# Performance work log

Hardware: AMD Instinct MI355X
Metric: run time of the kernel (lower is better)

## Reference

```python
import jax, jax.numpy as jnp
import numpy as np
import math

E = 512; V = 8192; B = 32; T = 16; L = 4; FF = 2048; NH = 8; TEMP = 1.0


def setup_inputs() -> dict:
    key = jax.random.key(0)
    ks = jax.random.split(key, 16)
    s = 0.02
    nrm = lambda k, shape, sc=s: jax.random.normal(k, shape, jnp.float32) * sc
    d = {}
    d['encoder_state'] = nrm(ks[0], (1, B, E), 1.0)
    d['special_symbol'] = nrm(ks[1], (1, 1, E))
    d['embed_weight'] = nrm(ks[2], (V, E), E ** -0.5)
    d['out_w'] = nrm(ks[3], (V, E))
    d['out_b'] = jnp.zeros((V,), jnp.float32)
    u = jax.random.uniform(ks[4], (T, B, V), jnp.float32, 1e-6, 1.0 - 1e-6)
    d['gumbel'] = -jnp.log(-jnp.log(u))
    d['sa_qkv_w'] = nrm(ks[5], (L, 3 * E, E)); d['sa_qkv_b'] = jnp.zeros((L, 3 * E), jnp.float32)
    d['sa_out_w'] = nrm(ks[6], (L, E, E)); d['sa_out_b'] = jnp.zeros((L, E), jnp.float32)
    d['ca_qkv_w'] = nrm(ks[7], (L, 3 * E, E)); d['ca_qkv_b'] = jnp.zeros((L, 3 * E), jnp.float32)
    d['ca_out_w'] = nrm(ks[8], (L, E, E)); d['ca_out_b'] = jnp.zeros((L, E), jnp.float32)
    for i in (1, 2, 3):
        d['ln%d_g' % i] = jnp.ones((L, E), jnp.float32)
        d['ln%d_b' % i] = jnp.zeros((L, E), jnp.float32)
    d['w1'] = nrm(ks[9], (L, FF, E)); d['b1'] = jnp.zeros((L, FF), jnp.float32)
    d['w2'] = nrm(ks[10], (L, E, FF)); d['b2'] = jnp.zeros((L, E), jnp.float32)
    return d


def _ln(x, g, b):
    m = x.mean(-1, keepdims=True)
    v = ((x - m) ** 2).mean(-1, keepdims=True)
    return (x - m) / jnp.sqrt(v + 1e-5) * g + b


def _mha(q_in, kv_in, qkv_w, qkv_b, out_w, out_b, mask):
    # q_in: [Sq,B,E], kv_in: [Sk,B,E]; fused PyTorch-style in_proj
    hd = E // NH
    wq, wk, wv = jnp.split(qkv_w, 3, 0)
    bq, bk, bv = jnp.split(qkv_b, 3, 0)
    q = (q_in @ wq.T + bq).reshape(q_in.shape[0], -1, NH, hd)
    k = (kv_in @ wk.T + bk).reshape(kv_in.shape[0], -1, NH, hd)
    v = (kv_in @ wv.T + bv).reshape(kv_in.shape[0], -1, NH, hd)
    s = jnp.einsum('qbhd,kbhd->bhqk', q, k) / math.sqrt(hd)
    if mask is not None:
        s = s + mask
    a = jax.nn.softmax(s, -1)
    o = jnp.einsum('bhqk,kbhd->qbhd', a, v).reshape(q_in.shape[0], -1, E)
    return o @ out_w.T + out_b


def _forward(encoder_state, special_symbol, embed_weight, out_w, out_b, gumbel,
             sa_qkv_w, sa_qkv_b, sa_out_w, sa_out_b,
             ca_qkv_w, ca_qkv_b, ca_out_w, ca_out_b,
             ln1_g, ln1_b, ln2_g, ln2_b, ln3_g, ln3_b,
             w1, b1, w2, b2):
    bsz = encoder_state.shape[1]
    embed_scale = math.sqrt(E)
    inp = jnp.broadcast_to(special_symbol, (1, bsz, E))  # special start symbol
    seq_steps, distribs = [], []
    for step in range(T):
        t = step + 1
        mask = jnp.where(jnp.triu(jnp.ones((t, t), bool), 1), -jnp.inf, 0.0)
        x = inp
        for l in range(L):  # post-norm TransformerDecoderLayer, erf-gelu
            sa = _mha(x, x, sa_qkv_w[l], sa_qkv_b[l], sa_out_w[l], sa_out_b[l], mask)
            x = _ln(x + sa, ln1_g[l], ln1_b[l])
            ca = _mha(x, encoder_state, ca_qkv_w[l], ca_qkv_b[l], ca_out_w[l], ca_out_b[l], None)
            x = _ln(x + ca, ln2_g[l], ln2_b[l])
            ff = jax.nn.gelu(x @ w1[l].T + b1[l], approximate=False) @ w2[l].T + b2[l]
            x = _ln(x + ff, ln3_g[l], ln3_b[l])
        logits = x[-1] @ out_w.T + out_b  # [B,V], last position only
        distribs.append(jax.nn.softmax(logits, -1))
        sample = jax.nn.softmax((logits + gumbel[step]) / TEMP, -1)  # gumbel-softmax (training mode)
        seq_steps.append(sample)
        new_emb = (sample @ embed_weight) * embed_scale  # soft embedding lookup
        inp = jnp.concatenate([inp, new_emb[None]], 0)
    sequence = jnp.stack(seq_steps).transpose(1, 0, 2)  # [B,T,V]
    eos = jnp.zeros_like(sequence[:, :1, :]).at[:, :, 0].set(1.0)
    sequence = jnp.concatenate([sequence, eos], 1)  # [B,T+1,V]
    return sequence, jnp.stack(distribs)  # distribs: [T,B,V]


def reference(encoder_state, special_symbol, embed_weight, out_w, out_b, gumbel,
              sa_qkv_w, sa_qkv_b, sa_out_w, sa_out_b,
              ca_qkv_w, ca_qkv_b, ca_out_w, ca_out_b,
              ln1_g, ln1_b, ln2_g, ln2_b, ln3_g, ln3_b,
              w1, b1, w2, b2):
    return _forward(encoder_state, special_symbol, embed_weight, out_w, out_b, gumbel,
                    sa_qkv_w, sa_qkv_b, sa_out_w, sa_out_b,
                    ca_qkv_w, ca_qkv_b, ca_out_w, ca_out_b,
                    ln1_g, ln1_b, ln2_g, ln2_b, ln3_g, ln3_b,
                    w1, b1, w2, b2)
```

## Files before the change

kernel.cpp:

```cpp
#include <hip/hip_runtime.h>
#include <math.h>

#define BB 32
#define EE 512
#define VV 8192
#define TT 16
#define LL 4
#define FFD 2048
#define NHD 8
#define HDD 64
#define LDP 520
#define RWP 516
#define OLP 72
#define SCALE_EMB 22.627416997969522f

typedef __attribute__((ext_vector_type(8))) short bf16x8;
typedef __attribute__((ext_vector_type(4))) float f32x4;
typedef unsigned long long ull;

__device__ __forceinline__ f32x4 mfma16(bf16x8 a, bf16x8 b, f32x4 c){
  return __builtin_amdgcn_mfma_f32_16x16x32_bf16(a, b, c, 0, 0, 0);
}

__device__ __forceinline__ float wave_sum(float v){
  for (int o = 32; o; o >>= 1) v += __shfl_down(v, o);
  return __shfl(v, 0);
}
__device__ __forceinline__ unsigned short f_to_bf(float f){
  unsigned u = __float_as_uint(f);
  unsigned r = (u + 0x7fffu + ((u >> 16) & 1u)) >> 16;
  return (unsigned short)r;
}
__device__ __forceinline__ float2 bf2_to_f2(const unsigned short* p){
  unsigned u = *(const unsigned*)p;
  float2 r;
  r.x = __uint_as_float(u << 16);
  r.y = __uint_as_float(u & 0xffff0000u);
  return r;
}
union UF { ull u; unsigned short s[4]; };
__device__ __forceinline__ ull pkbf4(float a, float b, float c, float d){
  UF x; x.s[0] = f_to_bf(a); x.s[1] = f_to_bf(b); x.s[2] = f_to_bf(c); x.s[3] = f_to_bf(d); return x.u;
}

__device__ __forceinline__ void gemm_chunk(const float* __restrict__ wrow0, int ldw,
    const unsigned short* xs, float* wt, float acc[4][2]){
  const int t = threadIdx.x, fg = t & 15, bg = t >> 4;
  #pragma unroll 1
  for (int c = 0; c < 8; ++c){
    const int k0 = c*64;
    __syncthreads();
    {
      int i = t*4;
      #pragma unroll
      for (int p = 0; p < 4; ++p, i += 1024){
        const int fr = i >> 6, kk = i & 63;
        float4 v = *(const float4*)(wrow0 + (size_t)fr*ldw + k0 + kk);
        wt[(kk+0)*68 + fr] = v.x;
        wt[(kk+1)*68 + fr] = v.y;
        wt[(kk+2)*68 + fr] = v.z;
        wt[(kk+3)*68 + fr] = v.w;
      }
    }
    __syncthreads();
    const unsigned short* xr0 = xs + (bg*2)*EE + k0;
    const unsigned short* xr1 = xr0 + EE;
    #pragma unroll 8
    for (int k = 0; k < 64; k += 2){
      float w0[4], w1[4];
      *(float4*)w0 = *(const float4*)(wt + (k+0)*68 + fg*4);
      *(float4*)w1 = *(const float4*)(wt + (k+1)*68 + fg*4);
      float2 xv0 = bf2_to_f2(xr0 + k);
      float2 xv1 = bf2_to_f2(xr1 + k);
      #pragma unroll
      for (int i = 0; i < 4; ++i){
        acc[i][0] += w0[i]*xv0.x + w1[i]*xv0.y;
        acc[i][1] += w0[i]*xv1.x + w1[i]*xv1.y;
      }
    }
  }
}

__device__ __forceinline__ void stage_x_512(unsigned short* xs,
    const float* __restrict__ xraw, const float* __restrict__ ybuf,
    const float* __restrict__ g, const float* __restrict__ bt, int use_ln,
    float* __restrict__ xlnout){
  if (!use_ln){
    for (int i = threadIdx.x*4; i < BB*EE; i += 2048){
      float4 v = *(const float4*)(xraw + i);
      int r = i >> 9, c = i & 511;
      *(ull*)(xs + r*LDP + c) = pkbf4(v.x, v.y, v.z, v.w);
    }
  } else {
    const int lane = threadIdx.x & 63, wv = threadIdx.x >> 6;
    for (int r = wv*4; r < wv*4 + 4; ++r){
      float vals[8]; float s = 0.f, s2 = 0.f;
      #pragma unroll
      for (int j = 0; j < 8; ++j){
        float v = ybuf[r*EE + lane + j*64];
        vals[j] = v; s += v; s2 += v*v;
      }
      s = wave_sum(s); s2 = wave_sum(s2);
      float m = s * (1.f/EE);
      float inv = rsqrtf(s2*(1.f/EE) - m*m + 1e-5f);
      #pragma unroll
      for (int j = 0; j < 8; ++j){
        int c = lane + j*64;
        float v = (vals[j]-m)*inv*g[c] + bt[c];
        xs[r*LDP + c] = f_to_bf(v);
        if (xlnout) xlnout[r*EE + c] = v;
      }
    }
  }
  __syncthreads();
}


__global__ __launch_bounds__(256) void k_init(const float* __restrict__ special,
    float* __restrict__ dseq, float* __restrict__ x,
    float* __restrict__ o2a, float* __restrict__ o2b,
    float* __restrict__ y0, float* __restrict__ y1){
  int idx = blockIdx.x*256 + threadIdx.x;
  if (idx < BB*VV){
    int b = idx >> 13, v = idx & (VV-1);
    dseq[(size_t)b*((TT+1)*VV) + (size_t)TT*VV + v] = (v == 0) ? 1.f : 0.f;
  } else if (idx < BB*VV + BB*EE){
    x[idx - BB*VV] = special[idx & (EE-1)];
  } else if (idx < BB*VV + 2*BB*EE){
    o2a[idx - BB*VV - BB*EE] = 0.f;
  } else if (idx < BB*VV + 3*BB*EE){
    o2b[idx - BB*VV - 2*BB*EE] = 0.f;
  } else if (idx < BB*VV + 4*BB*EE){
    y0[idx - BB*VV - 3*BB*EE] = 0.f;
  } else if (idx < BB*VV + 5*BB*EE){
    y1[idx - BB*VV - 4*BB*EE] = 0.f;
  }
}

__global__ __launch_bounds__(256) void k_penc(const float* __restrict__ enc,
    const float* __restrict__ w, const float* __restrict__ bias, float* __restrict__ venc){
  __shared__ unsigned short xs[BB*EE];
  __shared__ float wt[64*68];
  const int l = blockIdx.x >> 3, et = blockIdx.x & 7;
  for (int i = threadIdx.x; i < BB*EE; i += 256) xs[i] = f_to_bf(enc[i]);
  const int t = threadIdx.x, fg = t & 15, bg = t >> 4;
  const int f0 = et*64;
  const float* wl = w + (size_t)l*3*EE*EE + (size_t)(2*EE + f0)*EE;
  const float* bl = bias + l*3*EE + 2*EE + f0;
  float acc[4][2];
  #pragma unroll
  for (int i = 0; i < 4; ++i){ float bv = bl[fg*4+i]; acc[i][0] = bv; acc[i][1] = bv; }
  gemm_chunk(wl, EE, xs, wt, acc);
  #pragma unroll
  for (int i = 0; i < 4; ++i)
    #pragma unroll
    for (int j = 0; j < 2; ++j)
      venc[(size_t)l*BB*EE + (bg*2+j)*EE + f0 + fg*4 + i] = acc[i][j];
}

__global__ __launch_bounds__(256) void k_pca(const float* __restrict__ venc,
    const float* __restrict__ w, const float* __restrict__ bias, float* __restrict__ cac){
  __shared__ unsigned short xs[BB*EE];
  __shared__ float wt[64*68];
  const int l = blockIdx.x >> 3, et = blockIdx.x & 7;
  const float* vin = venc + (size_t)l*BB*EE;
  for (int i = threadIdx.x; i < BB*EE; i += 256) xs[i] = f_to_bf(vin[i]);
  const int t = threadIdx.x, fg = t & 15, bg = t >> 4;
  const int f0 = et*64;
  const float* wl = w + (size_t)l*EE*EE + (size_t)f0*EE;
  const float* bl = bias + l*EE + f0;
  float acc[4][2];
  #pragma unroll
  for (int i = 0; i < 4; ++i){ float bv = bl[fg*4+i]; acc[i][0] = bv; acc[i][1] = bv; }
  gemm_chunk(wl, EE, xs, wt, acc);
  #pragma unroll
  for (int i = 0; i < 4; ++i)
    #pragma unroll
    for (int j = 0; j < 2; ++j)
      cac[(size_t)l*BB*EE + (bg*2+j)*EE + f0 + fg*4 + i] = acc[i][j];
}

__global__ __launch_bounds__(256) void k_cvt(const float* __restrict__ s,
    unsigned short* __restrict__ d, int n4){
  int i = blockIdx.x*256 + threadIdx.x;
  if (i < n4){
    float4 v = ((const float4*)s)[i];
    ushort4 o;
    o.x = f_to_bf(v.x); o.y = f_to_bf(v.y); o.z = f_to_bf(v.z); o.w = f_to_bf(v.w);
    ((ushort4*)d)[i] = o;
  }
}

__global__ __launch_bounds__(256) void k_embT(const float* __restrict__ emb,
    unsigned short* __restrict__ eT){
  __shared__ unsigned short tl[64][68];
  const int vt = blockIdx.x >> 3, et = blockIdx.x & 7;
  const int v0 = vt*64, e0 = et*64;
  for (int i = threadIdx.x; i < 64*64; i += 256){
    int vv = i >> 6, ee = i & 63;
    tl[vv][ee] = f_to_bf(emb[(size_t)(v0+vv)*EE + e0 + ee]);
  }
  __syncthreads();
  for (int i = threadIdx.x; i < 64*64; i += 256){
    int ee = i >> 6, vv = i & 63;
    eT[(size_t)(e0+ee)*VV + v0 + vv] = tl[vv][ee];
  }
}


__global__ __launch_bounds__(512) void k_A(
    const float* __restrict__ x, const float* __restrict__ ybuf,
    const float* __restrict__ lng, const float* __restrict__ lnb, int use_ln,
    const unsigned short* __restrict__ Wb, const float* __restrict__ bias,
    const unsigned short* __restrict__ owb_l,
    float* __restrict__ kcl, float* __restrict__ vcl,
    float* __restrict__ xln, float* __restrict__ o2,
    int tpos, int tlen){
  __shared__ unsigned short xs[BB*LDP];
  __shared__ __align__(16) float qs[BB*68];
  __shared__ float att[BB*16];
  const int h = blockIdx.x;
  stage_x_512(xs, x, ybuf, lng, lnb, use_ln, (use_ln && h == 0) ? xln : nullptr);
  const int t = threadIdx.x, wv = t >> 6, lane = t & 63;
  const int lm = lane & 15, kg = lane >> 4;
  const unsigned short* b0r = xs + lm*LDP + kg*8;
  const unsigned short* b1r = xs + (lm+16)*LDP + kg*8;
  if (wv < 6){
    const int c = wv >> 1, half = wv & 1;
    #pragma unroll
    for (int ft = 0; ft < 2; ++ft){
      const int frel_t = (half*2 + ft)*16;
      const unsigned short* ar = Wb + (size_t)(c*EE + h*64 + frel_t + lm)*EE + kg*8;
      f32x4 acc0 = {0.f,0.f,0.f,0.f}, acc1 = {0.f,0.f,0.f,0.f};
      #pragma unroll 4
      for (int ks = 0; ks < 16; ++ks){
        bf16x8 a  = *reinterpret_cast<const bf16x8*>(ar + ks*32);
        bf16x8 b0 = *reinterpret_cast<const bf16x8*>(b0r + ks*32);
        bf16x8 b1 = *reinterpret_cast<const bf16x8*>(b1r + ks*32);
        acc0 = mfma16(a, b0, acc0);
        acc1 = mfma16(a, b1, acc1);
      }
      #pragma unroll
      for (int r = 0; r < 4; ++r){
        const int frel = frel_t + kg*4 + r;
        const float bv = bias[c*EE + h*64 + frel];
        float v0 = acc0[r] + bv, v1 = acc1[r] + bv;
        if (c == 0){
          qs[lm*68 + frel] = v0;
          qs[(lm+16)*68 + frel] = v1;
        } else if (c == 1){
          kcl[((lm*NHD + h)*TT + tpos)*HDD + frel] = v0;
          kcl[(((lm+16)*NHD + h)*TT + tpos)*HDD + frel] = v1;
        } else {
          vcl[((lm*NHD + h)*TT + tpos)*HDD + frel] = v0;
          vcl[(((lm+16)*NHD + h)*TT + tpos)*HDD + frel] = v1;
        }
      }
    }
  }
  __syncthreads();
  {
    const int b = t >> 4, j = t & 15;
    if (j < tlen){
      const float* qrow = qs + b*68;
      const float* krow = kcl + ((b*NHD + h)*TT + j)*HDD;
      float a = 0.f;
      #pragma unroll
      for (int d = 0; d < HDD; d += 4){
        float4 qv = *(const float4*)(qrow + d);
        float4 kv = *(const float4*)(krow + d);
        a += qv.x*kv.x + qv.y*kv.y + qv.z*kv.z + qv.w*kv.w;
      }
      att[b*16 + j] = a*0.125f;
    }
  }
  __syncthreads();
  if (t < 32){
    const int b = t;
    float m = -1e30f;
    for (int j = 0; j < tlen; ++j) m = fmaxf(m, att[b*16 + j]);
    float s = 0.f;
    for (int j = 0; j < tlen; ++j) s += __expf(att[b*16 + j] - m);
    float inv = 1.f/s;
    for (int j = 0; j < tlen; ++j) att[b*16 + j] = __expf(att[b*16 + j] - m)*inv;
  }
  __syncthreads();
  unsigned short* o_lds = (unsigned short*)qs;
  {
    const int b = t >> 4, d0 = (t & 15)*4;
    float acc[4];
    #pragma unroll
    for (int i = 0; i < 4; ++i) acc[i] = 0.f;
    const float* vrow = vcl + ((b*NHD + h)*TT)*HDD + d0;
    for (int j = 0; j < tlen; ++j){
      const float a = att[b*16 + j];
      float4 v = *(const float4*)(vrow + j*HDD);
      acc[0] += a*v.x; acc[1] += a*v.y; acc[2] += a*v.z; acc[3] += a*v.w;
    }
    *(ull*)(o_lds + b*OLP + d0) = pkbf4(acc[0], acc[1], acc[2], acc[3]);
  }
  __syncthreads();
  const unsigned short* ob0 = o_lds + lm*OLP + kg*8;
  const unsigned short* ob1 = o_lds + (lm+16)*OLP + kg*8;
  #pragma unroll
  for (int ft = 0; ft < 4; ++ft){
    const int f0 = wv*64 + ft*16;
    const unsigned short* ar = owb_l + (size_t)(f0 + lm)*EE + h*HDD + kg*8;
    f32x4 a0 = {0.f,0.f,0.f,0.f}, a1 = {0.f,0.f,0.f,0.f};
    #pragma unroll
    for (int ks = 0; ks < 2; ++ks){
      bf16x8 a  = *reinterpret_cast<const bf16x8*>(ar + ks*32);
      bf16x8 x0 = *reinterpret_cast<const bf16x8*>(ob0 + ks*32);
      bf16x8 x1 = *reinterpret_cast<const bf16x8*>(ob1 + ks*32);
      a0 = mfma16(a, x0, a0);
      a1 = mfma16(a, x1, a1);
    }
    #pragma unroll
    for (int r = 0; r < 4; ++r){
      const int f = f0 + kg*4 + r;
      atomicAdd(&o2[lm*EE + f], a0[r]);
      atomicAdd(&o2[(lm+16)*EE + f], a1[r]);
    }
  }
}

__global__ __launch_bounds__(512) void k_BC(
    const float* __restrict__ o2buf, const float* __restrict__ resid,
    const float* __restrict__ ob, const float* __restrict__ cac,
    const float* __restrict__ g1, const float* __restrict__ b1g,
    const float* __restrict__ g2, const float* __restrict__ b2g,
    const float* __restrict__ b2bias,
    const unsigned short* __restrict__ w1b, const float* __restrict__ b1bias,
    const unsigned short* __restrict__ w2b,
    float* __restrict__ ycur, float* __restrict__ yzero, float* __restrict__ o2zero){
  __shared__ unsigned short xs[BB*LDP];
  __shared__ __align__(16) float rawf[BB*RWP];
  __shared__ unsigned short Hs[BB*OLP];
  const int t = threadIdx.x, blk = blockIdx.x;
  for (int i = t*4; i < BB*EE; i += 2048){
    const int r = i >> 9, c = i & 511;
    float4 a  = *(const float4*)(o2buf + i);
    float4 rr = *(const float4*)(resid + i);
    float4 ov = *(const float4*)(ob + c);
    rawf[r*RWP + c]     = a.x + rr.x + ov.x;
    rawf[r*RWP + c + 1] = a.y + rr.y + ov.y;
    rawf[r*RWP + c + 2] = a.z + rr.z + ov.z;
    rawf[r*RWP + c + 3] = a.w + rr.w + ov.w;
  }
  __syncthreads();
  const int wv = t >> 6, lane = t & 63;
  const int lm = lane & 15, kg = lane >> 4;
  {
    const int c0 = lane*4, c1 = 256 + lane*4;
    for (int r = wv*4; r < wv*4 + 4; ++r){
      float v[8];
      *(float4*)(v+0) = *(const float4*)(rawf + r*RWP + c0);
      *(float4*)(v+4) = *(const float4*)(rawf + r*RWP + c1);
      float s = 0.f, s2 = 0.f;
      #pragma unroll
      for (int j = 0; j < 8; ++j){ s += v[j]; s2 += v[j]*v[j]; }
      s = wave_sum(s); s2 = wave_sum(s2);
      float m = s*(1.f/EE), inv = rsqrtf(s2*(1.f/EE) - m*m + 1e-5f);
      float4 ca0 = *(const float4*)(cac + (size_t)r*EE + c0);
      float4 ca1 = *(const float4*)(cac + (size_t)r*EE + c1);
      float nv[8]; float u = 0.f, u2 = 0.f;
      nv[0] = (v[0]-m)*inv*g1[c0+0] + b1g[c0+0] + ca0.x;
      nv[1] = (v[1]-m)*inv*g1[c0+1] + b1g[c0+1] + ca0.y;
      nv[2] = (v[2]-m)*inv*g1[c0+2] + b1g[c0+2] + ca0.z;
      nv[3] = (v[3]-m)*inv*g1[c0+3] + b1g[c0+3] + ca0.w;
      nv[4] = (v[4]-m)*inv*g1[c1+0] + b1g[c1+0] + ca1.x;
      nv[5] = (v[5]-m)*inv*g1[c1+1] + b1g[c1+1] + ca1.y;
      nv[6] = (v[6]-m)*inv*g1[c1+2] + b1g[c1+2] + ca1.z;
      nv[7] = (v[7]-m)*inv*g1[c1+3] + b1g[c1+3] + ca1.w;
      #pragma unroll
      for (int j = 0; j < 8; ++j){ u += nv[j]; u2 += nv[j]*nv[j]; }
      u = wave_sum(u); u2 = wave_sum(u2);
      float m2 = u*(1.f/EE), inv2 = rsqrtf(u2*(1.f/EE) - m2*m2 + 1e-5f);
      float o0 = (nv[0]-m2)*inv2*g2[c0+0] + b2g[c0+0];
      float o1 = (nv[1]-m2)*inv2*g2[c0+1] + b2g[c0+1];
      float o2v = (nv[2]-m2)*inv2*g2[c0+2] + b2g[c0+2];
      float o3 = (nv[3]-m2)*inv2*g2[c0+3] + b2g[c0+3];
      float o4 = (nv[4]-m2)*inv2*g2[c1+0] + b2g[c1+0];
      float o5 = (nv[5]-m2)*inv2*g2[c1+1] + b2g[c1+1];
      float o6 = (nv[6]-m2)*inv2*g2[c1+2] + b2g[c1+2];
      float o7 = (nv[7]-m2)*inv2*g2[c1+3] + b2g[c1+3];
      *(ull*)(xs + r*LDP + c0) = pkbf4(o0, o1, o2v, o3);
      *(ull*)(xs + r*LDP + c1) = pkbf4(o4, o5, o6, o7);
      if ((c0 >> 4) == blk){
        atomicAdd(&ycur[(size_t)r*EE + c0+0], o0 + b2bias[c0+0]);
        atomicAdd(&ycur[(size_t)r*EE + c0+1], o1 + b2bias[c0+1]);
        atomicAdd(&ycur[(size_t)r*EE + c0+2], o2v + b2bias[c0+2]);
        atomicAdd(&ycur[(size_t)r*EE + c0+3], o3 + b2bias[c0+3]);
      }
      if ((c1 >> 4) == blk){
        atomicAdd(&ycur[(size_t)r*EE + c1+0], o4 + b2bias[c1+0]);
        atomicAdd(&ycur[(size_t)r*EE + c1+1], o5 + b2bias[c1+1]);
        atomicAdd(&ycur[(size_t)r*EE + c1+2], o6 + b2bias[c1+2]);
        atomicAdd(&ycur[(size_t)r*EE + c1+3], o7 + b2bias[c1+3]);
      }
    }
  }
  __syncthreads();
  {
    const int ftile = wv & 3, rh = wv >> 2;
    const int f0w = blk*64 + ftile*16;
    const unsigned short* ar = w1b + (size_t)(f0w + lm)*EE + kg*8;
    const unsigned short* br = xs + (lm + rh*16)*LDP + kg*8;
    f32x4 acc = {0.f,0.f,0.f,0.f};
    #pragma unroll 4
    for (int ks = 0; ks < 16; ++ks){
      bf16x8 a = *reinterpret_cast<const bf16x8*>(ar + ks*32);
      bf16x8 b = *reinterpret_cast<const bf16x8*>(br + ks*32);
      acc = mfma16(a, b, acc);
    }
    const int fbrel = ftile*16 + kg*4;
    float hh[4];
    #pragma unroll
    for (int r = 0; r < 4; ++r){
      const float bv = b1bias[blk*64 + fbrel + r];
      float vv = acc[r] + bv;
      hh[r] = 0.5f*vv*(1.f + erff(vv*0.70710678118654752f));
    }
    *(ull*)(Hs + (lm + rh*16)*OLP + fbrel) = pkbf4(hh[0], hh[1], hh[2], hh[3]);
  }
  __syncthreads();
  {
    const unsigned short* hb0 = Hs + lm*OLP + kg*8;
    const unsigned short* hb1 = Hs + (lm+16)*OLP + kg*8;
    #pragma unroll
    for (int et = 0; et < 4; ++et){
      const int e0 = (wv*4 + et)*16;
      const unsigned short* ar = w2b + (size_t)(e0 + lm)*FFD + blk*64 + kg*8;
      f32x4 a0 = {0.f,0.f,0.f,0.f}, a1 = {0.f,0.f,0.f,0.f};
      #pragma unroll
      for (int ks = 0; ks < 2; ++ks){
        bf16x8 a  = *reinterpret_cast<const bf16x8*>(ar + ks*32);
        bf16x8 h0 = *reinterpret_cast<const bf16x8*>(hb0 + ks*32);
        bf16x8 h1 = *reinterpret_cast<const bf16x8*>(hb1 + ks*32);
        a0 = mfma16(a, h0, a0);
        a1 = mfma16(a, h1, a1);
      }
      #pragma unroll
      for (int r = 0; r < 4; ++r){
        const int e = e0 + kg*4 + r;
        atomicAdd(&ycur[lm*EE + e], a0[r]);
        atomicAdd(&ycur[(lm+16)*EE + e], a1[r]);
      }
    }
  }
  yzero[blk*512 + t] = 0.f;
  o2zero[blk*512 + t] = 0.f;
}

__global__ __launch_bounds__(512) void k_logits_m(
    const float* __restrict__ ybuf, const float* __restrict__ lng, const float* __restrict__ lnb,
    const unsigned short* __restrict__ Wb, const float* __restrict__ bias,
    float* __restrict__ logits){
  __shared__ unsigned short xs[BB*LDP];
  stage_x_512(xs, nullptr, ybuf, lng, lnb, 1, nullptr);
  const int t = threadIdx.x, wv = t >> 6, lane = t & 63;
  const int lm = lane & 15, kg = lane >> 4;
  const int ftile = wv & 3, rh = wv >> 2;
  const int f0w = blockIdx.x*64 + ftile*16;
  const unsigned short* ar = Wb + (size_t)(f0w + lm)*EE + kg*8;
  const unsigned short* br = xs + (lm + rh*16)*LDP + kg*8;
  f32x4 acc = {0.f,0.f,0.f,0.f};
  #pragma unroll 4
  for (int ks = 0; ks < 16; ++ks){
    bf16x8 a = *reinterpret_cast<const bf16x8*>(ar + ks*32);
    bf16x8 b = *reinterpret_cast<const bf16x8*>(br + ks*32);
    acc = mfma16(a, b, acc);
  }
  #pragma unroll
  for (int r = 0; r < 4; ++r){
    const int f = f0w + kg*4 + r;
    logits[(size_t)(lm + rh*16)*VV + f] = acc[r] + bias[f];
  }
}

__global__ __launch_bounds__(512) void k_softmax(const float* __restrict__ logits,
    const float* __restrict__ gum, float* __restrict__ dseq, float* __restrict__ ddist,
    unsigned short* __restrict__ sbf, float* __restrict__ x, int step){
  const int b = blockIdx.x, t = threadIdx.x, lane = t & 63, wv = t >> 6;
  __shared__ float red[16];
  const float* lr = logits + (size_t)b*VV;
  const float* gr = gum + (size_t)b*VV;
  float lv[16], gv[16];
  #pragma unroll
  for (int g4 = 0; g4 < 4; ++g4){
    const int i0 = t*4 + g4*2048;
    float4 l4 = *(const float4*)(lr + i0);
    float4 g4v = *(const float4*)(gr + i0);
    lv[g4*4+0]=l4.x; lv[g4*4+1]=l4.y; lv[g4*4+2]=l4.z; lv[g4*4+3]=l4.w;
    gv[g4*4+0]=g4v.x; gv[g4*4+1]=g4v.y; gv[g4*4+2]=g4v.z; gv[g4*4+3]=g4v.w;
  }
  float m1 = -1e30f, m2 = -1e30f;
  #pragma unroll
  for (int j = 0; j < 16; ++j){
    m1 = fmaxf(m1, lv[j]);
    m2 = fmaxf(m2, lv[j] + gv[j]);
  }
  for (int o = 32; o; o >>= 1){ m1 = fmaxf(m1, __shfl_down(m1,o)); m2 = fmaxf(m2, __shfl_down(m2,o)); }
  if (lane == 0){ red[wv] = m1; red[8+wv] = m2; }
  __syncthreads();
  m1 = red[0]; m2 = red[8];
  #pragma unroll
  for (int j = 1; j < 8; ++j){ m1 = fmaxf(m1, red[j]); m2 = fmaxf(m2, red[8+j]); }
  __syncthreads();
  float s1 = 0.f, s2 = 0.f;
  #pragma unroll
  for (int j = 0; j < 16; ++j){
    s1 += __expf(lv[j] - m1);
    s2 += __expf(lv[j] + gv[j] - m2);
  }
  for (int o = 32; o; o >>= 1){ s1 += __shfl_down(s1,o); s2 += __shfl_down(s2,o); }
  if (lane == 0){ red[wv] = s1; red[8+wv] = s2; }
  __syncthreads();
  s1 = 0.f; s2 = 0.f;
  #pragma unroll
  for (int j = 0; j < 8; ++j){ s1 += red[j]; s2 += red[8+j]; }
  float r1 = 1.f/s1, r2 = 1.f/s2;
  float* dq = dseq + (size_t)b*((TT+1)*VV) + (size_t)step*VV;
  float* dd = ddist + (size_t)b*VV;
  #pragma unroll
  for (int g4 = 0; g4 < 4; ++g4){
    const int i0 = t*4 + g4*2048;
    float4 ddv, dqv;
    ddv.x = __expf(lv[g4*4+0]-m1)*r1; ddv.y = __expf(lv[g4*4+1]-m1)*r1;
    ddv.z = __expf(lv[g4*4+2]-m1)*r1; ddv.w = __expf(lv[g4*4+3]-m1)*r1;
    dqv.x = __expf(lv[g4*4+0]+gv[g4*4+0]-m2)*r2;
    dqv.y = __expf(lv[g4*4+1]+gv[g4*4+1]-m2)*r2;
    dqv.z = __expf(lv[g4*4+2]+gv[g4*4+2]-m2)*r2;
    dqv.w = __expf(lv[g4*4+3]+gv[g4*4+3]-m2)*r2;
    *(float4*)(dd + i0) = ddv;
    *(float4*)(dq + i0) = dqv;
    *(ull*)(sbf + (size_t)b*VV + i0) = pkbf4(dqv.x, dqv.y, dqv.z, dqv.w);
  }
  x[b*EE + t] = 0.f;
}

__global__ __launch_bounds__(512) void k_embed_m(
    const unsigned short* __restrict__ eT, const unsigned short* __restrict__ sbf,
    float* __restrict__ x){
  const int t = threadIdx.x, wv = t >> 6, lane = t & 63;
  const int lm = lane & 15, kg = lane >> 4;
  const int etile = wv & 3, rh = wv >> 2;
  const int e0 = (blockIdx.x & 7)*64 + etile*16;
  const int v0 = (blockIdx.x >> 3)*512;
  const unsigned short* ar = eT + (size_t)(e0 + lm)*VV + v0 + kg*8;
  const unsigned short* br = sbf + (size_t)(lm + rh*16)*VV + v0 + kg*8;
  f32x4 acc = {0.f,0.f,0.f,0.f};
  #pragma unroll 4
  for (int ks = 0; ks < 16; ++ks){
    bf16x8 a = *reinterpret_cast<const bf16x8*>(ar + ks*32);
    bf16x8 b = *reinterpret_cast<const bf16x8*>(br + ks*32);
    acc = mfma16(a, b, acc);
  }
  #pragma unroll
  for (int r = 0; r < 4; ++r){
    const int e = e0 + kg*4 + r;
    atomicAdd(&x[(lm + rh*16)*EE + e], acc[r]*SCALE_EMB);
  }
}

extern "C" void kernel_launch(void* const* d_in, const int* in_sizes, int n_in,
                              void* d_out, int out_size, void* d_ws, size_t ws_size,
                              hipStream_t stream){
  (void)in_sizes; (void)n_in; (void)out_size; (void)ws_size;
  const float* enc  = (const float*)d_in[0];
  const float* spec = (const float*)d_in[1];
  const float* embw = (const float*)d_in[2];
  const float* outw = (const float*)d_in[3];
  const float* outb = (const float*)d_in[4];
  const float* gumb = (const float*)d_in[5];
  const float* saqw = (const float*)d_in[6];
  const float* saqb = (const float*)d_in[7];
  const float* saow = (const float*)d_in[8];
  const float* saob = (const float*)d_in[9];
  const float* caqw = (const float*)d_in[10];
  const float* caqb = (const float*)d_in[11];
  const float* caow = (const float*)d_in[12];
  const float* caob = (const float*)d_in[13];
  const float* l1g  = (const float*)d_in[14];
  const float* l1b  = (const float*)d_in[15];
  const float* l2g  = (const float*)d_in[16];
  const float* l2b  = (const float*)d_in[17];
  const float* l3g  = (const float*)d_in[18];
  const float* l3b  = (const float*)d_in[19];
  const float* w1   = (const float*)d_in[20];
  const float* b1   = (const float*)d_in[21];
  const float* w2   = (const float*)d_in[22];
  const float* b2   = (const float*)d_in[23];

  float* dout = (float*)d_out;
  float* dseq = dout;
  float* ddistbase = dout + (size_t)BB*(TT+1)*VV;

  unsigned char* p = (unsigned char*)d_ws;
  auto alloc = [&](size_t bytes) -> void* {
    void* r = (void*)p; p += (bytes + 255) & ~(size_t)255; return r;
  };
  float* x      = (float*)alloc(BB*EE*4);
  float* y0     = (float*)alloc(BB*EE*4);
  float* y1     = (float*)alloc(BB*EE*4);
  float* xln    = (float*)alloc(BB*EE*4);
  float* o2a    = (float*)alloc(BB*EE*4);
  float* o2b    = (float*)alloc(BB*EE*4);
  float* logits = (float*)alloc((size_t)BB*VV*4);
  float* venc   = (float*)alloc((size_t)LL*BB*EE*4);
  float* cac    = (float*)alloc((size_t)LL*BB*EE*4);
  float* kcache = (float*)alloc((size_t)LL*BB*EE*TT*4);
  float* vcache = (float*)alloc((size_t)LL*BB*EE*TT*4);
  unsigned short* sbf   = (unsigned short*)alloc((size_t)BB*VV*2);
  unsigned short* wqkvb = (unsigned short*)alloc((size_t)LL*3*EE*EE*2);
  unsigned short* owb   = (unsigned short*)alloc((size_t)LL*EE*EE*2);
  unsigned short* w1b   = (unsigned short*)alloc((size_t)LL*FFD*EE*2);
  unsigned short* w2b   = (unsigned short*)alloc((size_t)LL*FFD*EE*2);
  unsigned short* outwb = (unsigned short*)alloc((size_t)VV*EE*2);
  unsigned short* eTb   = (unsigned short*)alloc((size_t)EE*VV*2);

  k_init<<<1344, 256, 0, stream>>>(spec, dseq, x, o2a, o2b, y0, y1);
  k_penc<<<32, 256, 0, stream>>>(enc, caqw, caqb, venc);
  k_pca<<<32, 256, 0, stream>>>(venc, caow, caob, cac);
  k_cvt<<<(LL*3*EE*EE/4 + 255)/256, 256, 0, stream>>>(saqw, wqkvb, LL*3*EE*EE/4);
  k_cvt<<<(LL*EE*EE/4 + 255)/256, 256, 0, stream>>>(saow, owb, LL*EE*EE/4);
  k_cvt<<<(LL*FFD*EE/4 + 255)/256, 256, 0, stream>>>(w1, w1b, LL*FFD*EE/4);
  k_cvt<<<(LL*FFD*EE/4 + 255)/256, 256, 0, stream>>>(w2, w2b, LL*FFD*EE/4);
  k_cvt<<<(VV*EE/4 + 255)/256, 256, 0, stream>>>(outw, outwb, VV*EE/4);
  k_embT<<<1024, 256, 0, stream>>>(embw, eTb);

  float* yb[2]  = { y0, y1 };
  float* o2p[2] = { o2a, o2b };

  for (int step = 0; step < TT; ++step){
    const int tpos = step, tlen = step + 1;
    for (int l = 0; l < LL; ++l){
      const int use_ln = (l > 0);
      const int par = l & 1, opp = par ^ 1;
      const float* lg = l3g + (use_ln ? (l-1)*EE : 0);
      const float* lb = l3b + (use_ln ? (l-1)*EE : 0);
      float* kcl = kcache + (size_t)l*BB*EE*TT;
      float* vcl = vcache + (size_t)l*BB*EE*TT;
      k_A<<<NHD, 512, 0, stream>>>(x, yb[opp], lg, lb, use_ln,
          wqkvb + (size_t)l*3*EE*EE, saqb + (size_t)l*3*EE,
          owb + (size_t)l*EE*EE, kcl, vcl, xln, o2p[par], tpos, tlen);
      k_BC<<<32, 512, 0, stream>>>(o2p[par], use_ln ? xln : x,
          saob + (size_t)l*EE, cac + (size_t)l*BB*EE,
          l1g + l*EE, l1b + l*EE, l2g + l*EE, l2b + l*EE, b2 + l*EE,
          w1b + (size_t)l*FFD*EE, b1 + l*FFD, w2b + (size_t)l*EE*FFD,
          yb[par], yb[opp], o2p[opp]);
    }
    k_logits_m<<<128, 512, 0, stream>>>(yb[1], l3g + 3*EE, l3b + 3*EE, outwb, outb, logits);
    k_softmax<<<32, 512, 0, stream>>>(logits, gumb + (size_t)step*BB*VV, dseq,
        ddistbase + (size_t)step*BB*VV, sbf, x, step);
    k_embed_m<<<128, 512, 0, stream>>>(eTb, sbf, x);
  }
}
```

Measured before the change: 4.143 ms.

## Fuse softmax into logits and embedding kernels using unshifted exponent sums

The separate softmax kernel is removed. The logits kernel now computes exp(logit) and exp(logit+gumbel) directly, with no max subtraction, writes both to buffers and accumulates the row sums atomically. A combined kernel then normalizes, runs the soft embedding matmul, and writes the distribution and sequence outputs. Zeroing of x and gs moves into the layer kernels. This saves one launch per step and the round trip through the logits buffer, but without the max shift exp can overflow when logits are large, and global float atomics make the sums order-dependent.

```diff
diff --git a/kernel.cpp b/kernel.cpp
--- a/kernel.cpp
+++ b/kernel.cpp
@@ -215,13 +215,15 @@
     const unsigned short* __restrict__ owb_l,
     float* __restrict__ kcl, float* __restrict__ vcl,
     float* __restrict__ xln, float* __restrict__ o2,
-    int tpos, int tlen){
+    float* __restrict__ gs, int tpos, int tlen){
   __shared__ unsigned short xs[BB*LDP];
   __shared__ __align__(16) float qs[BB*68];
   __shared__ float att[BB*16];
   const int h = blockIdx.x;
+  const int t = threadIdx.x;
+  if (!use_ln && h == 0 && t < 64) gs[t] = 0.f;
   stage_x_512(xs, x, ybuf, lng, lnb, use_ln, (use_ln && h == 0) ? xln : nullptr);
-  const int t = threadIdx.x, wv = t >> 6, lane = t & 63;
+  const int wv = t >> 6, lane = t & 63;
   const int lm = lane & 15, kg = lane >> 4;
   const unsigned short* b0r = xs + lm*LDP + kg*8;
   const unsigned short* b1r = xs + (lm+16)*LDP + kg*8;
@@ -332,7 +334,8 @@
     const float* __restrict__ b2bias,
     const unsigned short* __restrict__ w1b, const float* __restrict__ b1bias,
     const unsigned short* __restrict__ w2b,
-    float* __restrict__ ycur, float* __restrict__ yzero, float* __restrict__ o2zero){
+    float* __restrict__ ycur, float* __restrict__ yzero, float* __restrict__ o2zero,
+    float* __restrict__ xz){
   __shared__ unsigned short xs[BB*LDP];
   __shared__ __align__(16) float rawf[BB*RWP];
   __shared__ unsigned short Hs[BB*OLP];
@@ -450,20 +453,74 @@
   }
   yzero[blk*512 + t] = 0.f;
   o2zero[blk*512 + t] = 0.f;
-}
-
-__global__ __launch_bounds__(512) void k_logits_m(
+  if (xz) xz[blk*512 + t] = 0.f;
+}
+
+__global__ __launch_bounds__(512) void k_logits_e(
     const float* __restrict__ ybuf, const float* __restrict__ lng, const float* __restrict__ lnb,
     const unsigned short* __restrict__ Wb, const float* __restrict__ bias,
-    float* __restrict__ logits){
+    const float* __restrict__ gum,
+    float* __restrict__ el, float* __restrict__ eg, float* __restrict__ gs){
   __shared__ unsigned short xs[BB*LDP];
+  __shared__ float ls[64];
+  const int t = threadIdx.x;
+  if (t < 64) ls[t] = 0.f;
   stage_x_512(xs, nullptr, ybuf, lng, lnb, 1, nullptr);
-  const int t = threadIdx.x, wv = t >> 6, lane = t & 63;
+  const int wv = t >> 6, lane = t & 63;
   const int lm = lane & 15, kg = lane >> 4;
   const int ftile = wv & 3, rh = wv >> 2;
   const int f0w = blockIdx.x*64 + ftile*16;
+  const int b = lm + rh*16;
   const unsigned short* ar = Wb + (size_t)(f0w + lm)*EE + kg*8;
-  const unsigned short* br = xs + (lm + rh*16)*LDP + kg*8;
+  const unsigned short* br = xs + b*LDP + kg*8;
+  f32x4 acc = {0.f,0.f,0.f,0.f};
+  #pragma unroll 4
+  for (int ks = 0; ks < 16; ++ks){
+    bf16x8 a = *reinterpret_cast<const bf16x8*>(ar + ks*32);
+    bf16x8 bb = *reinterpret_cast<const bf16x8*>(br + ks*32);
+    acc = mfma16(a, bb, acc);
+  }
+  const int fb = f0w + kg*4;
+  float4 g4 = *(const float4*)(gum + (size_t)b*VV + fb);
+  float l0 = acc[0] + bias[fb+0], l1 = acc[1] + bias[fb+1];
+  float l2 = acc[2] + bias[fb+2], l3 = acc[3] + bias[fb+3];
+  float e10 = __expf(l0), e11 = __expf(l1), e12 = __expf(l2), e13 = __expf(l3);
+  float e20 = __expf(l0+g4.x), e21 = __expf(l1+g4.y), e22 = __expf(l2+g4.z), e23 = __expf(l3+g4.w);
+  float4 ev1; ev1.x=e10; ev1.y=e11; ev1.z=e12; ev1.w=e13;
+  float4 ev2; ev2.x=e20; ev2.y=e21; ev2.z=e22; ev2.w=e23;
+  *(float4*)(el + (size_t)b*VV + fb) = ev1;
+  *(float4*)(eg + (size_t)b*VV + fb) = ev2;
+  atomicAdd(&ls[b],      e10+e11+e12+e13);
+  atomicAdd(&ls[32 + b], e20+e21+e22+e23);
+  __syncthreads();
+  if (t < 64) atomicAdd(&gs[t], ls[t]);
+}
+
+__global__ __launch_bounds__(512) void k_SMEM(
+    const unsigned short* __restrict__ eT,
+    const float* __restrict__ el, const float* __restrict__ eg,
+    const float* __restrict__ gs,
+    float* __restrict__ dseq, float* __restrict__ ddist,
+    float* __restrict__ x, int step){
+  __shared__ unsigned short ss[BB*LDP];
+  __shared__ float rr[64];
+  const int t = threadIdx.x;
+  const int et = blockIdx.x & 7, v0 = (blockIdx.x >> 3)*512;
+  if (t < 64) rr[t] = 1.f / gs[t];
+  __syncthreads();
+  for (int i = t*4; i < BB*512; i += 2048){
+    const int r = i >> 9, c = i & 511;
+    float4 e4 = *(const float4*)(eg + (size_t)r*VV + v0 + c);
+    const float r2v = rr[32 + r];
+    *(ull*)(ss + r*LDP + c) = pkbf4(e4.x*r2v, e4.y*r2v, e4.z*r2v, e4.w*r2v);
+  }
+  __syncthreads();
+  const int wv = t >> 6, lane = t & 63;
+  const int lm = lane & 15, kg = lane >> 4;
+  const int etile = wv & 3, rh = wv >> 2;
+  const int e0 = et*64 + etile*16;
+  const unsigned short* ar = eT + (size_t)(e0 + lm)*VV + v0 + kg*8;
+  const unsigned short* br = ss + (lm + rh*16)*LDP + kg*8;
   f32x4 acc = {0.f,0.f,0.f,0.f};
   #pragma unroll 4
   for (int ks = 0; ks < 16; ++ks){
@@ -473,93 +530,20 @@
   }
   #pragma unroll
   for (int r = 0; r < 4; ++r){
-    const int f = f0w + kg*4 + r;
-    logits[(size_t)(lm + rh*16)*VV + f] = acc[r] + bias[f];
-  }
-}
-
-__global__ __launch_bounds__(512) void k_softmax(const float* __restrict__ logits,
-    const float* __restrict__ gum, float* __restrict__ dseq, float* __restrict__ ddist,
-    unsigned short* __restrict__ sbf, float* __restrict__ x, int step){
-  const int b = blockIdx.x, t = threadIdx.x, lane = t & 63, wv = t >> 6;
-  __shared__ float red[16];
-  const float* lr = logits + (size_t)b*VV;
-  const float* gr = gum + (size_t)b*VV;
-  float lv[16], gv[16];
-  #pragma unroll
-  for (int g4 = 0; g4 < 4; ++g4){
-    const int i0 = t*4 + g4*2048;
-    float4 l4 = *(const float4*)(lr + i0);
-    float4 g4v = *(const float4*)(gr + i0);
-    lv[g4*4+0]=l4.x; lv[g4*4+1]=l4.y; lv[g4*4+2]=l4.z; lv[g4*4+3]=l4.w;
-    gv[g4*4+0]=g4v.x; gv[g4*4+1]=g4v.y; gv[g4*4+2]=g4v.z; gv[g4*4+3]=g4v.w;
-  }
-  float m1 = -1e30f, m2 = -1e30f;
-  #pragma unroll
-  for (int j = 0; j < 16; ++j){
-    m1 = fmaxf(m1, lv[j]);
-    m2 = fmaxf(m2, lv[j] + gv[j]);
-  }
-  for (int o = 32; o; o >>= 1){ m1 = fmaxf(m1, __shfl_down(m1,o)); m2 = fmaxf(m2, __shfl_down(m2,o)); }
-  if (lane == 0){ red[wv] = m1; red[8+wv] = m2; }
-  __syncthreads();
-  m1 = red[0]; m2 = red[8];
-  #pragma unroll
-  for (int j = 1; j < 8; ++j){ m1 = fmaxf(m1, red[j]); m2 = fmaxf(m2, red[8+j]); }
-  __syncthreads();
-  float s1 = 0.f, s2 = 0.f;
-  #pragma unroll
-  for (int j = 0; j < 16; ++j){
-    s1 += __expf(lv[j] - m1);
-    s2 += __expf(lv[j] + gv[j] - m2);
-  }
-  for (int o = 32; o; o >>= 1){ s1 += __shfl_down(s1,o); s2 += __shfl_down(s2,o); }
-  if (lane == 0){ red[wv] = s1; red[8+wv] = s2; }
-  __syncthreads();
-  s1 = 0.f; s2 = 0.f;
-  #pragma unroll
-  for (int j = 0; j < 8; ++j){ s1 += red[j]; s2 += red[8+j]; }
-  float r1 = 1.f/s1, r2 = 1.f/s2;
-  float* dq = dseq + (size_t)b*((TT+1)*VV) + (size_t)step*VV;
-  float* dd = ddist + (size_t)b*VV;
-  #pragma unroll
-  for (int g4 = 0; g4 < 4; ++g4){
-    const int i0 = t*4 + g4*2048;
-    float4 ddv, dqv;
-    ddv.x = __expf(lv[g4*4+0]-m1)*r1; ddv.y = __expf(lv[g4*4+1]-m1)*r1;
-    ddv.z = __expf(lv[g4*4+2]-m1)*r1; ddv.w = __expf(lv[g4*4+3]-m1)*r1;
-    dqv.x = __expf(lv[g4*4+0]+gv[g4*4+0]-m2)*r2;
-    dqv.y = __expf(lv[g4*4+1]+gv[g4*4+1]-m2)*r2;
-    dqv.z = __expf(lv[g4*4+2]+gv[g4*4+2]-m2)*r2;
-    dqv.w = __expf(lv[g4*4+3]+gv[g4*4+3]-m2)*r2;
-    *(float4*)(dd + i0) = ddv;
-    *(float4*)(dq + i0) = dqv;
-    *(ull*)(sbf + (size_t)b*VV + i0) = pkbf4(dqv.x, dqv.y, dqv.z, dqv.w);
-  }
-  x[b*EE + t] = 0.f;
-}
-
-__global__ __launch_bounds__(512) void k_embed_m(
-    const unsigned short* __restrict__ eT, const unsigned short* __restrict__ sbf,
-    float* __restrict__ x){
-  const int t = threadIdx.x, wv = t >> 6, lane = t & 63;
-  const int lm = lane & 15, kg = lane >> 4;
-  const int etile = wv & 3, rh = wv >> 2;
-  const int e0 = (blockIdx.x & 7)*64 + etile*16;
-  const int v0 = (blockIdx.x >> 3)*512;
-  const unsigned short* ar = eT + (size_t)(e0 + lm)*VV + v0 + kg*8;
-  const unsigned short* br = sbf + (size_t)(lm + rh*16)*VV + v0 + kg*8;
-  f32x4 acc = {0.f,0.f,0.f,0.f};
-  #pragma unroll 4
-  for (int ks = 0; ks < 16; ++ks){
-    bf16x8 a = *reinterpret_cast<const bf16x8*>(ar + ks*32);
-    bf16x8 b = *reinterpret_cast<const bf16x8*>(br + ks*32);
-    acc = mfma16(a, b, acc);
-  }
-  #pragma unroll
-  for (int r = 0; r < 4; ++r){
     const int e = e0 + kg*4 + r;
     atomicAdd(&x[(lm + rh*16)*EE + e], acc[r]*SCALE_EMB);
+  }
+  if (et == 0){
+    for (int i = t*4; i < BB*512; i += 2048){
+      const int r = i >> 9, c = i & 511;
+      float4 e2 = *(const float4*)(eg + (size_t)r*VV + v0 + c);
+      float4 e1 = *(const float4*)(el + (size_t)r*VV + v0 + c);
+      const float r1v = rr[r], r2v = rr[32 + r];
+      float4 dq; dq.x=e2.x*r2v; dq.y=e2.y*r2v; dq.z=e2.z*r2v; dq.w=e2.w*r2v;
+      float4 dd; dd.x=e1.x*r1v; dd.y=e1.y*r1v; dd.z=e1.z*r1v; dd.w=e1.w*r1v;
+      *(float4*)(dseq + (size_t)r*((TT+1)*VV) + (size_t)step*VV + v0 + c) = dq;
+      *(float4*)(ddist + (size_t)r*VV + v0 + c) = dd;
+    }
   }
 }
 
@@ -606,12 +590,13 @@
   float* xln    = (float*)alloc(BB*EE*4);
   float* o2a    = (float*)alloc(BB*EE*4);
   float* o2b    = (float*)alloc(BB*EE*4);
-  float* logits = (float*)alloc((size_t)BB*VV*4);
+  float* el     = (float*)alloc((size_t)BB*VV*4);
+  float* eg     = (float*)alloc((size_t)BB*VV*4);
+  float* gs     = (float*)alloc(64*4);
   float* venc   = (float*)alloc((size_t)LL*BB*EE*4);
   float* cac    = (float*)alloc((size_t)LL*BB*EE*4);
   float* kcache = (float*)alloc((size_t)LL*BB*EE*TT*4);
   float* vcache = (float*)alloc((size_t)LL*BB*EE*TT*4);
-  unsigned short* sbf   = (unsigned short*)alloc((size_t)BB*VV*2);
   unsigned short* wqkvb = (unsigned short*)alloc((size_t)LL*3*EE*EE*2);
   unsigned short* owb   = (unsigned short*)alloc((size_t)LL*EE*EE*2);
   unsigned short* w1b   = (unsigned short*)alloc((size_t)LL*FFD*EE*2);
@@ -643,16 +628,16 @@
       float* vcl = vcache + (size_t)l*BB*EE*TT;
       k_A<<<NHD, 512, 0, stream>>>(x, yb[opp], lg, lb, use_ln,
           wqkvb + (size_t)l*3*EE*EE, saqb + (size_t)l*3*EE,
-          owb + (size_t)l*EE*EE, kcl, vcl, xln, o2p[par], tpos, tlen);
+          owb + (size_t)l*EE*EE, kcl, vcl, xln, o2p[par], gs, tpos, tlen);
       k_BC<<<32, 512, 0, stream>>>(o2p[par], use_ln ? xln : x,
           saob + (size_t)l*EE, cac + (size_t)l*BB*EE,
           l1g + l*EE, l1b + l*EE, l2g + l*EE, l2b + l*EE, b2 + l*EE,
           w1b + (size_t)l*FFD*EE, b1 + l*FFD, w2b + (size_t)l*EE*FFD,
-          yb[par], yb[opp], o2p[opp]);
-    }
-    k_logits_m<<<128, 512, 0, stream>>>(yb[1], l3g + 3*EE, l3b + 3*EE, outwb, outb, logits);
-    k_softmax<<<32, 512, 0, stream>>>(logits, gumb + (size_t)step*BB*VV, dseq,
-        ddistbase + (size_t)step*BB*VV, sbf, x, step);
-    k_embed_m<<<128, 512, 0, stream>>>(eTb, sbf, x);
-  }
-}
+          yb[par], yb[opp], o2p[opp], (l == 1) ? x : nullptr);
+    }
+    k_logits_e<<<128, 512, 0, stream>>>(yb[1], l3g + 3*EE, l3b + 3*EE, outwb, outb,
+        gumb + (size_t)step*BB*VV, el, eg, gs);
+    k_SMEM<<<128, 512, 0, stream>>>(eTb, el, eg, gs, dseq,
+        ddistbase + (size_t)step*BB*VV, x, step);
+  }
+}
```

Measured after the change: 4.163 ms. No clear change (+0.5%).
